# Optimization experiments

Measured on AMD Instinct MI355X. Metric: run time of the kernel, lower is better.

## Reference

```python
import jax, jax.numpy as jnp
import numpy as np

R = 32768          # number of human-object pairs
IN_FEATS = 3072    # input_size * 3 (person + object + union features)
HIDDEN = 1024      # input_size
NUM_CLASSES = 50   # action classes


def setup_inputs() -> dict:
    key = jax.random.key(0)
    k_x, k_w1, k_w2 = jax.random.split(key, 3)
    x = jax.random.normal(k_x, (R, IN_FEATS), dtype=jnp.float32)
    # Linear weights init: normal(std=0.01), bias 0 (as in the module)
    w1 = jax.random.normal(k_w1, (IN_FEATS, HIDDEN), dtype=jnp.float32) * 0.01
    b1 = jnp.zeros((HIDDEN,), dtype=jnp.float32)
    w2 = jax.random.normal(k_w2, (HIDDEN, NUM_CLASSES), dtype=jnp.float32) * 0.01
    b2 = jnp.zeros((NUM_CLASSES,), dtype=jnp.float32)
    return {"x": x, "w1": w1, "b1": b1, "w2": w2, "b2": b2}


def reference(x, w1, b1, w2, b2):
    # HoiOutputLayers.forward: scores = cls_score(relu(cls_fc1(x)))
    h = jax.nn.relu(jnp.dot(x, w1) + b1)          # [R, HIDDEN]
    scores = jnp.dot(h, w2) + b2                  # [R, NUM_CLASSES] action logits
    return scores
```

## Files before the change

### kernel.cpp

```cpp
#include <hip/hip_runtime.h>

#define K1 3072
#define N1 1024
#define NCOL 50

typedef float  f32x4  __attribute__((ext_vector_type(4)));
typedef short  short8 __attribute__((ext_vector_type(8)));

#define GLD16(g, l)                                                        \
  __builtin_amdgcn_global_load_lds(                                        \
      (const __attribute__((address_space(1))) void*)(g),                  \
      (__attribute__((address_space(3))) void*)(l), 16, 0, 0)

#define MFMA_BF16(a, b, c) __builtin_amdgcn_mfma_f32_16x16x32_bf16(a, b, c, 0, 0, 0)

__device__ inline unsigned bfr(float f) {
  return (__builtin_bit_cast(unsigned, f) + 0x8000u) >> 16;
}
__device__ inline short f2bf(float f) { return (short)bfr(f); }
__device__ inline short8 cvt8(float4 a, float4 b) {
  short8 r;
  r[0] = f2bf(a.x); r[1] = f2bf(a.y); r[2] = f2bf(a.z); r[3] = f2bf(a.w);
  r[4] = f2bf(b.x); r[5] = f2bf(b.y); r[6] = f2bf(b.z); r[7] = f2bf(b.w);
  return r;
}

__global__ __launch_bounds__(512) void xcvt_kernel(const float* __restrict__ X,
                                                   short* __restrict__ Xb) {
  size_t i = ((size_t)blockIdx.x * 512 + threadIdx.x) * 8;
  const size_t stride = (size_t)2048 * 512 * 8;
#pragma unroll 4
  for (int it = 0; it < 12; ++it, i += stride) {
    float4 u = *(const float4*)(X + i);
    float4 v = *(const float4*)(X + i + 4);
    *(short8*)(Xb + i) = cvt8(u, v);
  }
}

__global__ __launch_bounds__(256) void w1t_kernel(const float* __restrict__ W1,
                                                  short* __restrict__ W1T) {
  __shared__ float tile[64 * 65];
  const int t = threadIdx.x, b = blockIdx.x;
  const int k0 = (b >> 4) * 64, n0 = (b & 15) * 64;
#pragma unroll
  for (int i = 0; i < 16; ++i) {
    const int e = t + i * 256, r = e >> 6, c = e & 63;
    tile[r * 65 + c] = W1[(size_t)(k0 + r) * N1 + n0 + c];
  }
  __syncthreads();
#pragma unroll
  for (int i = 0; i < 16; ++i) {
    const int e = t + i * 256, kx = e & 63, ny = e >> 6;
    W1T[(size_t)(n0 + ny) * K1 + k0 + kx] = f2bf(tile[kx * 65 + ny]);
  }
}

__global__ __launch_bounds__(256) void w2t_kernel(const float* __restrict__ W2,
                                                  short* __restrict__ W2T) {
  const int idx = blockIdx.x * 256 + threadIdx.x;
  for (int e = idx; e < 64 * N1; e += 16 * 256) {
    const int c = e >> 10, k = e & 1023;
    const float v = (c < NCOL) ? W2[(size_t)k * NCOL + c] : 0.f;
    W2T[(size_t)c * N1 + k] = f2bf(v);
  }
}

#define BK2 64
#define NIT (K1 / BK2)
#define ASLOT (256 * 64)
#define SH2 264

struct __align__(16) Smem2 {
  union {
    struct { short A[2][ASLOT]; short B[2][ASLOT]; } s;
    struct { short h[128 * SH2]; short w2t[64 * SH2]; } e;
  } u;
};

__global__ __launch_bounds__(512, 2)
void hoi_fused2(const short* __restrict__ Xb, const short* __restrict__ W1T,
                const float* __restrict__ B1, const short* __restrict__ W2T,
                const float* __restrict__ B2, float* __restrict__ OUT) {
  __shared__ Smem2 sm;
  const int tid  = threadIdx.x;
  const int lane = tid & 63, wid = tid >> 6;
  const int wr = wid >> 2, wc = wid & 3;
  const int l15 = lane & 15, g = lane >> 4, l7 = l15 & 7;

  const int bid  = blockIdx.x;
  const int gidx = (bid & 7) * 64 + (bid >> 3);
  const int m_blk = gidx >> 2, n_blk = gidx & 3;
  const int m0 = m_blk * 256, n0 = n_blk * 256;

  const int srow  = lane >> 3;
  const int sslot = (lane & 7) ^ srow;
  const short* aS0 = Xb  + (size_t)(m0 + 0   + wid * 16 + srow) * K1 + sslot * 8;
  const short* aS1 = Xb  + (size_t)(m0 + 128 + wid * 16 + srow) * K1 + sslot * 8;
  const short* bS0 = W1T + (size_t)(n0 + 0   + wid * 16 + srow) * K1 + sslot * 8;
  const short* bS1 = W1T + (size_t)(n0 + 128 + wid * 16 + srow) * K1 + sslot * 8;
  const int dL0 = (0   + wid * 16) * 64;
  const int dL1 = (128 + wid * 16) * 64;

#define ISSUE_A0(kt, sl) do { GLD16(aS0 + (size_t)(kt) * BK2,                  &sm.u.s.A[sl][dL0]);        \
                              GLD16(aS0 + (size_t)8 * K1 + (size_t)(kt) * BK2, &sm.u.s.A[sl][dL0 + 512]); } while (0)
#define ISSUE_A1(kt, sl) do { GLD16(aS1 + (size_t)(kt) * BK2,                  &sm.u.s.A[sl][dL1]);        \
                              GLD16(aS1 + (size_t)8 * K1 + (size_t)(kt) * BK2, &sm.u.s.A[sl][dL1 + 512]); } while (0)
#define ISSUE_B0(kt, sl) do { GLD16(bS0 + (size_t)(kt) * BK2,                  &sm.u.s.B[sl][dL0]);        \
                              GLD16(bS0 + (size_t)8 * K1 + (size_t)(kt) * BK2, &sm.u.s.B[sl][dL0 + 512]); } while (0)
#define ISSUE_B1(kt, sl) do { GLD16(bS1 + (size_t)(kt) * BK2,                  &sm.u.s.B[sl][dL1]);        \
                              GLD16(bS1 + (size_t)8 * K1 + (size_t)(kt) * BK2, &sm.u.s.B[sl][dL1 + 512]); } while (0)

  const int aRd = (wr * 128 + l15) * 64;
  const int bRd = (wc * 64  + l15) * 64;
  const int sk0 = ((g)     ^ l7) * 8;
  const int sk1 = ((4 | g) ^ l7) * 8;

  float b1v[4];
#pragma unroll
  for (int nf = 0; nf < 4; ++nf) b1v[nf] = B1[n0 + wc * 64 + nf * 16 + l15];

  f32x4 acc[8][4] = {};

  ISSUE_A0(0, 0); ISSUE_A1(0, 0); ISSUE_B0(0, 0); ISSUE_B1(0, 0);

  for (int t = 0; t < NIT; ++t) {
    const int s  = t & 1, sx = s ^ 1;
    const int tn = (t + 1 < NIT) ? t + 1 : NIT - 1;

    __builtin_amdgcn_s_barrier();
    ISSUE_A0(tn, sx);
    __builtin_amdgcn_sched_barrier(0);
    asm volatile("s_waitcnt vmcnt(2)" ::: "memory");
    __builtin_amdgcn_s_barrier();
    __builtin_amdgcn_sched_barrier(0);
    ISSUE_A1(tn, sx);
    ISSUE_B0(tn, sx);
    ISSUE_B1(tn, sx);
    __builtin_amdgcn_sched_barrier(0);

    short8 a_[4][2], b_[4][2];

#pragma unroll
    for (int mf = 0; mf < 4; ++mf) {
      a_[mf][0] = *(const short8*)&sm.u.s.A[s][aRd + mf * 1024 + sk0];
      a_[mf][1] = *(const short8*)&sm.u.s.A[s][aRd + mf * 1024 + sk1];
    }
#pragma unroll
    for (int nf = 0; nf < 2; ++nf) {
      b_[nf][0] = *(const short8*)&sm.u.s.B[s][bRd + nf * 1024 + sk0];
      b_[nf][1] = *(const short8*)&sm.u.s.B[s][bRd + nf * 1024 + sk1];
    }
    asm volatile("s_waitcnt lgkmcnt(0)" ::: "memory");
    __builtin_amdgcn_sched_barrier(0);
    __builtin_amdgcn_s_setprio(1);
#pragma unroll
    for (int mf = 0; mf < 4; ++mf)
#pragma unroll
      for (int nf = 0; nf < 2; ++nf) {
        acc[mf][nf] = MFMA_BF16(a_[mf][0], b_[nf][0], acc[mf][nf]);
        acc[mf][nf] = MFMA_BF16(a_[mf][1], b_[nf][1], acc[mf][nf]);
      }
    __builtin_amdgcn_s_setprio(0);
    __builtin_amdgcn_sched_barrier(0);

#pragma unroll
    for (int nf = 2; nf < 4; ++nf) {
      b_[nf][0] = *(const short8*)&sm.u.s.B[s][bRd + nf * 1024 + sk0];
      b_[nf][1] = *(const short8*)&sm.u.s.B[s][bRd + nf * 1024 + sk1];
    }
    asm volatile("s_waitcnt lgkmcnt(0)" ::: "memory");
    __builtin_amdgcn_sched_barrier(0);
    __builtin_amdgcn_s_setprio(1);
#pragma unroll
    for (int mf = 0; mf < 4; ++mf)
#pragma unroll
      for (int nf = 2; nf < 4; ++nf) {
        acc[mf][nf] = MFMA_BF16(a_[mf][0], b_[nf][0], acc[mf][nf]);
        acc[mf][nf] = MFMA_BF16(a_[mf][1], b_[nf][1], acc[mf][nf]);
      }
    __builtin_amdgcn_s_setprio(0);
    __builtin_amdgcn_sched_barrier(0);

#pragma unroll
    for (int mf = 0; mf < 4; ++mf) {
      a_[mf][0] = *(const short8*)&sm.u.s.A[s][aRd + (4 + mf) * 1024 + sk0];
      a_[mf][1] = *(const short8*)&sm.u.s.A[s][aRd + (4 + mf) * 1024 + sk1];
    }
    asm volatile("s_waitcnt lgkmcnt(0)" ::: "memory");
    __builtin_amdgcn_sched_barrier(0);
    __builtin_amdgcn_s_setprio(1);
#pragma unroll
    for (int mf = 0; mf < 4; ++mf)
#pragma unroll
      for (int nf = 0; nf < 2; ++nf) {
        acc[4 + mf][nf] = MFMA_BF16(a_[mf][0], b_[nf][0], acc[4 + mf][nf]);
        acc[4 + mf][nf] = MFMA_BF16(a_[mf][1], b_[nf][1], acc[4 + mf][nf]);
      }
    __builtin_amdgcn_s_setprio(0);
    __builtin_amdgcn_sched_barrier(0);

    __builtin_amdgcn_s_setprio(1);
#pragma unroll
    for (int mf = 0; mf < 4; ++mf)
#pragma unroll
      for (int nf = 2; nf < 4; ++nf) {
        acc[4 + mf][nf] = MFMA_BF16(a_[mf][0], b_[nf][0], acc[4 + mf][nf]);
        acc[4 + mf][nf] = MFMA_BF16(a_[mf][1], b_[nf][1], acc[4 + mf][nf]);
      }
    __builtin_amdgcn_s_setprio(0);
  }
#undef ISSUE_A0
#undef ISSUE_A1
#undef ISSUE_B0
#undef ISSUE_B1

  for (int ph = 0; ph < 2; ++ph) {
    __syncthreads();

    if (wr == ph) {
#pragma unroll
      for (int mf = 0; mf < 8; ++mf)
#pragma unroll
        for (int nf = 0; nf < 4; ++nf) {
          const int c = wc * 64 + nf * 16 + l15;
#pragma unroll
          for (int j = 0; j < 4; ++j) {
            const int r = mf * 16 + g * 4 + j;
            sm.u.e.h[r * SH2 + c] = f2bf(fmaxf(acc[mf][nf][j] + b1v[nf], 0.f));
          }
        }
    }
    if (ph == 0) {
      const int c = tid & 63, part = tid >> 6;
#pragma unroll
      for (int i = 0; i < 4; ++i)
        *(short8*)&sm.u.e.w2t[c * SH2 + part * 32 + i * 8] =
            *(const short8*)&W2T[(size_t)c * N1 + n0 + part * 32 + i * 8];
    }
    __syncthreads();

    f32x4 acc2[4] = {};
#pragma unroll
    for (int ks = 0; ks < 8; ++ks) {
      const short8 a2 = *(const short8*)&sm.u.e.h[(wid * 16 + l15) * SH2 + ks * 32 + g * 8];
#pragma unroll
      for (int nt = 0; nt < 4; ++nt) {
        const short8 b2 = *(const short8*)&sm.u.e.w2t[(nt * 16 + l15) * SH2 + ks * 32 + g * 8];
        acc2[nt] = MFMA_BF16(a2, b2, acc2[nt]);
      }
    }
#pragma unroll
    for (int nt = 0; nt < 4; ++nt) {
      const int c = nt * 16 + l15;
      if (c < NCOL) {
#pragma unroll
        for (int j = 0; j < 4; ++j) {
          const int r = m0 + ph * 128 + wid * 16 + g * 4 + j;
          float v = acc2[nt][j];
          if (n_blk == 0) v += B2[c];
          atomicAdd(&OUT[(size_t)r * NCOL + c], v);
        }
      }
    }
  }
}

#define BK 32
#define NSTEP (K1 / BK)
#define SAS 40
#define SHS 136

struct __align__(16) Smem0 {
  union {
    struct { short A[128 * SAS]; short BT[128 * SAS]; } s[2];
    struct { short h[64 * SHS]; short w2t[64 * SHS]; } e;
  } u;
};

__global__ __launch_bounds__(256, 3)
void hoi_fused0(const float* __restrict__ X, const float* __restrict__ W1,
                const float* __restrict__ B1, const float* __restrict__ W2,
                const float* __restrict__ B2, float* __restrict__ OUT) {
  __shared__ Smem0 sm;
  const int tid  = threadIdx.x;
  const int lane = tid & 63, wid = tid >> 6;
  const int wr = wid >> 1, wc = wid & 1;
  const int l15 = lane & 15, g = lane >> 4;
  const int bid   = blockIdx.x;
  const int xcd   = bid & 7, o = bid >> 3;
  const int m_blk = xcd * 32 + (o >> 3);
  const int n_blk = o & 7;
  const int m0 = m_blk * 128, n0 = n_blk * 128;

  const int arow = tid >> 1;
  const int akc  = (tid & 1) << 4;
  const float* aptr = X + (size_t)(m0 + arow) * K1 + akc;
  const int bk2 = tid >> 4, bcm = tid & 15;
  const float* bptr = W1 + (size_t)(2 * bk2) * N1 + n0 + bcm;

  float b1v[4];
#pragma unroll
  for (int nt = 0; nt < 4; ++nt) b1v[nt] = B1[n0 + wc * 64 + nt * 16 + l15];

  f32x4 acc[4][4] = {};
  float4 ra[4];
  float  rb0[8], rb1[8];
#pragma unroll
  for (int q = 0; q < 4; ++q) ra[q] = *(const float4*)(aptr + 4 * q);
#pragma unroll
  for (int i = 0; i < 8; ++i) { rb0[i] = bptr[16 * i]; rb1[i] = bptr[N1 + 16 * i]; }

  for (int step = 0; step < NSTEP; ++step) {
    const int cb = step & 1;
    const short8 av0 = cvt8(ra[0], ra[1]);
    const short8 av1 = cvt8(ra[2], ra[3]);
    unsigned bpk[8];
#pragma unroll
    for (int i = 0; i < 8; ++i)
      bpk[i] = bfr(rb0[i]) | ((__builtin_bit_cast(unsigned, rb1[i]) + 0x8000u) & 0xFFFF0000u);
    if (step + 1 < NSTEP) {
      const int k0v = (step + 1) * BK;
#pragma unroll
      for (int q = 0; q < 4; ++q) ra[q] = *(const float4*)(aptr + k0v + 4 * q);
      const float* bp = bptr + (size_t)k0v * N1;
#pragma unroll
      for (int i = 0; i < 8; ++i) { rb0[i] = bp[16 * i]; rb1[i] = bp[N1 + 16 * i]; }
    }
    *(short8*)&sm.u.s[cb].A[arow * SAS + akc + 0] = av0;
    *(short8*)&sm.u.s[cb].A[arow * SAS + akc + 8] = av1;
#pragma unroll
    for (int i = 0; i < 8; ++i)
      *(unsigned*)&sm.u.s[cb].BT[(bcm + 16 * i) * SAS + 2 * bk2] = bpk[i];

    asm volatile("s_waitcnt lgkmcnt(0)" ::: "memory");
    __builtin_amdgcn_s_barrier();
    __builtin_amdgcn_sched_barrier(0);

    short8 af[4];
#pragma unroll
    for (int mt = 0; mt < 4; ++mt)
      af[mt] = *(const short8*)&sm.u.s[cb].A[(wr * 64 + mt * 16 + l15) * SAS + g * 8];
#pragma unroll
    for (int nt = 0; nt < 4; ++nt) {
      short8 bfv = *(const short8*)&sm.u.s[cb].BT[(wc * 64 + nt * 16 + l15) * SAS + g * 8];
#pragma unroll
      for (int mt = 0; mt < 4; ++mt)
        acc[mt][nt] = MFMA_BF16(af[mt], bfv, acc[mt][nt]);
    }
  }

  for (int p = 0; p < 2; ++p) {
    __syncthreads();
    if (wr == p) {
#pragma unroll
      for (int mt = 0; mt < 4; ++mt)
#pragma unroll
        for (int nt = 0; nt < 4; ++nt) {
          const int c = wc * 64 + nt * 16 + l15;
#pragma unroll
          for (int j = 0; j < 4; ++j) {
            const int r = mt * 16 + g * 4 + j;
            sm.u.e.h[r * SHS + c] = f2bf(fmaxf(acc[mt][nt][j] + b1v[nt], 0.f));
          }
        }
    }
    if (p == 0) {
      const int kk = tid >> 1, ch = (tid & 1) * 32;
#pragma unroll
      for (int i = 0; i < 32; ++i) {
        const int c = ch + i;
        const float v = (c < NCOL) ? W2[(size_t)(n0 + kk) * NCOL + c] : 0.f;
        sm.u.e.w2t[c * SHS + kk] = f2bf(v);
      }
    }
    __syncthreads();

    f32x4 acc2[4] = {};
#pragma unroll
    for (int ks = 0; ks < 4; ++ks) {
      const short8 a2f = *(const short8*)&sm.u.e.h[(wid * 16 + l15) * SHS + ks * 32 + g * 8];
#pragma unroll
      for (int nt2 = 0; nt2 < 4; ++nt2) {
        const short8 b2f = *(const short8*)&sm.u.e.w2t[(nt2 * 16 + l15) * SHS + ks * 32 + g * 8];
        acc2[nt2] = MFMA_BF16(a2f, b2f, acc2[nt2]);
      }
    }
#pragma unroll
    for (int nt2 = 0; nt2 < 4; ++nt2) {
      const int c = nt2 * 16 + l15;
      if (c < NCOL) {
#pragma unroll
        for (int j = 0; j < 4; ++j) {
          const int r = m0 + p * 64 + wid * 16 + g * 4 + j;
          float v = acc2[nt2][j];
          if (n_blk == 0) v += B2[c];
          atomicAdd(&OUT[(size_t)r * NCOL + c], v);
        }
      }
    }
  }
}

extern "C" void kernel_launch(void* const* d_in, const int* in_sizes, int n_in,
                              void* d_out, int out_size, void* d_ws, size_t ws_size,
                              hipStream_t stream) {
  const float* X  = (const float*)d_in[0];
  const float* W1 = (const float*)d_in[1];
  const float* B1 = (const float*)d_in[2];
  const float* W2 = (const float*)d_in[3];
  const float* B2 = (const float*)d_in[4];
  float* OUT = (float*)d_out;

  const size_t XB_BYTES  = (size_t)32768 * K1 * 2;
  const size_t W1T_BYTES = (size_t)N1 * K1 * 2;
  const size_t W2T_BYTES = (size_t)64 * N1 * 2;

  hipMemsetAsync(d_out, 0, (size_t)out_size * sizeof(float), stream);

  if (ws_size >= XB_BYTES + W1T_BYTES + W2T_BYTES) {
    short* Xb  = (short*)d_ws;
    short* W1T = (short*)((char*)d_ws + XB_BYTES);
    short* W2T = (short*)((char*)d_ws + XB_BYTES + W1T_BYTES);
    hipLaunchKernelGGL(xcvt_kernel, dim3(2048), dim3(512), 0, stream, X, Xb);
    hipLaunchKernelGGL(w1t_kernel, dim3(768), dim3(256), 0, stream, W1, W1T);
    hipLaunchKernelGGL(w2t_kernel, dim3(16), dim3(256), 0, stream, W2, W2T);
    hipLaunchKernelGGL(hoi_fused2, dim3(512), dim3(512), 0, stream, Xb, W1T, B1, W2T, B2, OUT);
  } else {
    hipLaunchKernelGGL(hoi_fused0, dim3(2048), dim3(256), 0, stream, X, W1, B1, W2, B2, OUT);
  }
}
```

Before: 340.4 us.

## Interleave global-to-LDS prefetch issues across MFMA phases with finer barriers

Reassigns which rows each wave loads so the A and B tiles split into four quarter-chunks, each issued between the four MFMA phases of the main loop rather than all at the top of the iteration. Per-phase vmcnt waits and workgroup barriers are added so each chunk is known complete before the next iteration reads it. The aim is to spread memory issue evenly across compute and hide load latency behind MFMAs. The cost is many more s_barrier syncs per iteration, which could add stalls.

```diff
diff --git a/kernel.cpp b/kernel.cpp
--- a/kernel.cpp
+++ b/kernel.cpp
@@ -13,6 +13,7 @@
       (__attribute__((address_space(3))) void*)(l), 16, 0, 0)
 
 #define MFMA_BF16(a, b, c) __builtin_amdgcn_mfma_f32_16x16x32_bf16(a, b, c, 0, 0, 0)
+#define SBAR()  __builtin_amdgcn_sched_barrier(0)
 
 __device__ inline unsigned bfr(float f) {
   return (__builtin_bit_cast(unsigned, f) + 0x8000u) >> 16;
@@ -94,21 +95,26 @@
 
   const int srow  = lane >> 3;
   const int sslot = (lane & 7) ^ srow;
-  const short* aS0 = Xb  + (size_t)(m0 + 0   + wid * 16 + srow) * K1 + sslot * 8;
-  const short* aS1 = Xb  + (size_t)(m0 + 128 + wid * 16 + srow) * K1 + sslot * 8;
-  const short* bS0 = W1T + (size_t)(n0 + 0   + wid * 16 + srow) * K1 + sslot * 8;
-  const short* bS1 = W1T + (size_t)(n0 + 128 + wid * 16 + srow) * K1 + sslot * 8;
-  const int dL0 = (0   + wid * 16) * 64;
-  const int dL1 = (128 + wid * 16) * 64;
-
-#define ISSUE_A0(kt, sl) do { GLD16(aS0 + (size_t)(kt) * BK2,                  &sm.u.s.A[sl][dL0]);        \
-                              GLD16(aS0 + (size_t)8 * K1 + (size_t)(kt) * BK2, &sm.u.s.A[sl][dL0 + 512]); } while (0)
-#define ISSUE_A1(kt, sl) do { GLD16(aS1 + (size_t)(kt) * BK2,                  &sm.u.s.A[sl][dL1]);        \
-                              GLD16(aS1 + (size_t)8 * K1 + (size_t)(kt) * BK2, &sm.u.s.A[sl][dL1 + 512]); } while (0)
-#define ISSUE_B0(kt, sl) do { GLD16(bS0 + (size_t)(kt) * BK2,                  &sm.u.s.B[sl][dL0]);        \
-                              GLD16(bS0 + (size_t)8 * K1 + (size_t)(kt) * BK2, &sm.u.s.B[sl][dL0 + 512]); } while (0)
-#define ISSUE_B1(kt, sl) do { GLD16(bS1 + (size_t)(kt) * BK2,                  &sm.u.s.B[sl][dL1]);        \
-                              GLD16(bS1 + (size_t)8 * K1 + (size_t)(kt) * BK2, &sm.u.s.B[sl][dL1 + 512]); } while (0)
+
+  const int uj0 = 2 * wid, uj1 = 2 * wid + 1;
+  const int arA_0 = (uj0 >> 3) * 128 + (uj0 & 7) * 8;
+  const int arA_1 = (uj1 >> 3) * 128 + (uj1 & 7) * 8;
+  const int brB_0 = (uj0 >> 2) * 64 + (uj0 & 3) * 8;
+  const int brB_1 = (uj1 >> 2) * 64 + (uj1 & 3) * 8;
+
+  const short* aP0 = Xb  + (size_t)(m0 + arA_0 + srow) * K1 + sslot * 8;
+  const short* aP1 = Xb  + (size_t)(m0 + arA_1 + srow) * K1 + sslot * 8;
+  const short* bP0 = W1T + (size_t)(n0 + brB_0 + srow) * K1 + sslot * 8;
+  const short* bP1 = W1T + (size_t)(n0 + brB_1 + srow) * K1 + sslot * 8;
+
+#define ISSUE_A0(kt, sl) do { GLD16(aP0 + (size_t)(kt) * BK2,                   &sm.u.s.A[sl][arA_0 * 64]);        \
+                              GLD16(aP1 + (size_t)(kt) * BK2,                   &sm.u.s.A[sl][arA_1 * 64]); } while (0)
+#define ISSUE_A1(kt, sl) do { GLD16(aP0 + (size_t)64 * K1 + (size_t)(kt) * BK2, &sm.u.s.A[sl][arA_0 * 64 + 4096]); \
+                              GLD16(aP1 + (size_t)64 * K1 + (size_t)(kt) * BK2, &sm.u.s.A[sl][arA_1 * 64 + 4096]); } while (0)
+#define ISSUE_B0(kt, sl) do { GLD16(bP0 + (size_t)(kt) * BK2,                   &sm.u.s.B[sl][brB_0 * 64]);        \
+                              GLD16(bP1 + (size_t)(kt) * BK2,                   &sm.u.s.B[sl][brB_1 * 64]); } while (0)
+#define ISSUE_B1(kt, sl) do { GLD16(bP0 + (size_t)32 * K1 + (size_t)(kt) * BK2, &sm.u.s.B[sl][brB_0 * 64 + 2048]); \
+                              GLD16(bP1 + (size_t)32 * K1 + (size_t)(kt) * BK2, &sm.u.s.B[sl][brB_1 * 64 + 2048]); } while (0)
 
   const int aRd = (wr * 128 + l15) * 64;
   const int bRd = (wc * 64  + l15) * 64;
@@ -121,23 +127,18 @@
 
   f32x4 acc[8][4] = {};
 
-  ISSUE_A0(0, 0); ISSUE_A1(0, 0); ISSUE_B0(0, 0); ISSUE_B1(0, 0);
+  ISSUE_A0(0, 0); SBAR();
+  ISSUE_B0(0, 0); SBAR();
+  ISSUE_B1(0, 0); SBAR();
+  ISSUE_A1(0, 0); SBAR();
+  asm volatile("s_waitcnt vmcnt(4)" ::: "memory");
+  __builtin_amdgcn_s_barrier();
+  SBAR();
 
   for (int t = 0; t < NIT; ++t) {
     const int s  = t & 1, sx = s ^ 1;
     const int tn = (t + 1 < NIT) ? t + 1 : NIT - 1;
 
-    __builtin_amdgcn_s_barrier();
-    ISSUE_A0(tn, sx);
-    __builtin_amdgcn_sched_barrier(0);
-    asm volatile("s_waitcnt vmcnt(2)" ::: "memory");
-    __builtin_amdgcn_s_barrier();
-    __builtin_amdgcn_sched_barrier(0);
-    ISSUE_A1(tn, sx);
-    ISSUE_B0(tn, sx);
-    ISSUE_B1(tn, sx);
-    __builtin_amdgcn_sched_barrier(0);
-
     short8 a_[4][2], b_[4][2];
 
 #pragma unroll
@@ -150,8 +151,11 @@
       b_[nf][0] = *(const short8*)&sm.u.s.B[s][bRd + nf * 1024 + sk0];
       b_[nf][1] = *(const short8*)&sm.u.s.B[s][bRd + nf * 1024 + sk1];
     }
+    ISSUE_A0(tn, sx);
+    SBAR();
+    __builtin_amdgcn_s_barrier();
     asm volatile("s_waitcnt lgkmcnt(0)" ::: "memory");
-    __builtin_amdgcn_sched_barrier(0);
+    SBAR();
     __builtin_amdgcn_s_setprio(1);
 #pragma unroll
     for (int mf = 0; mf < 4; ++mf)
@@ -161,15 +165,21 @@
         acc[mf][nf] = MFMA_BF16(a_[mf][1], b_[nf][1], acc[mf][nf]);
       }
     __builtin_amdgcn_s_setprio(0);
-    __builtin_amdgcn_sched_barrier(0);
+    asm volatile("s_waitcnt vmcnt(4)" ::: "memory");
+    SBAR();
+    __builtin_amdgcn_s_barrier();
+    SBAR();
 
 #pragma unroll
     for (int nf = 2; nf < 4; ++nf) {
       b_[nf][0] = *(const short8*)&sm.u.s.B[s][bRd + nf * 1024 + sk0];
       b_[nf][1] = *(const short8*)&sm.u.s.B[s][bRd + nf * 1024 + sk1];
     }
+    ISSUE_B0(tn, sx);
+    SBAR();
+    __builtin_amdgcn_s_barrier();
     asm volatile("s_waitcnt lgkmcnt(0)" ::: "memory");
-    __builtin_amdgcn_sched_barrier(0);
+    SBAR();
     __builtin_amdgcn_s_setprio(1);
 #pragma unroll
     for (int mf = 0; mf < 4; ++mf)
@@ -179,15 +189,21 @@
         acc[mf][nf] = MFMA_BF16(a_[mf][1], b_[nf][1], acc[mf][nf]);
       }
     __builtin_amdgcn_s_setprio(0);
-    __builtin_amdgcn_sched_barrier(0);
+    asm volatile("s_waitcnt vmcnt(4)" ::: "memory");
+    SBAR();
+    __builtin_amdgcn_s_barrier();
+    SBAR();
 
 #pragma unroll
     for (int mf = 0; mf < 4; ++mf) {
       a_[mf][0] = *(const short8*)&sm.u.s.A[s][aRd + (4 + mf) * 1024 + sk0];
       a_[mf][1] = *(const short8*)&sm.u.s.A[s][aRd + (4 + mf) * 1024 + sk1];
     }
+    ISSUE_B1(tn, sx);
+    SBAR();
+    __builtin_amdgcn_s_barrier();
     asm volatile("s_waitcnt lgkmcnt(0)" ::: "memory");
-    __builtin_amdgcn_sched_barrier(0);
+    SBAR();
     __builtin_amdgcn_s_setprio(1);
 #pragma unroll
     for (int mf = 0; mf < 4; ++mf)
@@ -197,8 +213,13 @@
         acc[4 + mf][nf] = MFMA_BF16(a_[mf][1], b_[nf][1], acc[4 + mf][nf]);
       }
     __builtin_amdgcn_s_setprio(0);
-    __builtin_amdgcn_sched_barrier(0);
-
+    SBAR();
+    __builtin_amdgcn_s_barrier();
+    SBAR();
+
+    ISSUE_A1(tn, sx);
+    SBAR();
+    __builtin_amdgcn_s_barrier();
     __builtin_amdgcn_s_setprio(1);
 #pragma unroll
     for (int mf = 0; mf < 4; ++mf)
@@ -208,6 +229,10 @@
         acc[4 + mf][nf] = MFMA_BF16(a_[mf][1], b_[nf][1], acc[4 + mf][nf]);
       }
     __builtin_amdgcn_s_setprio(0);
+    asm volatile("s_waitcnt vmcnt(4)" ::: "memory");
+    SBAR();
+    __builtin_amdgcn_s_barrier();
+    SBAR();
   }
 #undef ISSUE_A0
 #undef ISSUE_A1
```

Measured after the change: 340.5 us. No clear change (+0.0%).

## Double waves per block and halve per-wave tile in fused HOI GEMM

Applied to the files above, without the earlier changes.

Launches the fused GEMM with 1024 threads (16 waves) instead of 512. The block still covers a 256x256 output tile, but each wave now owns a 64x64 sub-tile with half the accumulators. Global-to-LDS staging is redistributed so each wave issues one 16-byte load per operand half. The second-layer epilogue is split across more waves. The aim is more resident waves to hide memory and LDS latency, at the cost of more LDS fragment reads per MFMA and less register-level reuse.

```diff
diff --git a/kernel.cpp b/kernel.cpp
--- a/kernel.cpp
+++ b/kernel.cpp
@@ -13,6 +13,7 @@
       (__attribute__((address_space(3))) void*)(l), 16, 0, 0)
 
 #define MFMA_BF16(a, b, c) __builtin_amdgcn_mfma_f32_16x16x32_bf16(a, b, c, 0, 0, 0)
+#define SBAR()  __builtin_amdgcn_sched_barrier(0)
 
 __device__ inline unsigned bfr(float f) {
   return (__builtin_bit_cast(unsigned, f) + 0x8000u) >> 16;
@@ -77,8 +78,8 @@
   } u;
 };
 
-__global__ __launch_bounds__(512, 2)
-void hoi_fused2(const short* __restrict__ Xb, const short* __restrict__ W1T,
+__global__ __launch_bounds__(1024, 4)
+void hoi_fused3(const short* __restrict__ Xb, const short* __restrict__ W1T,
                 const float* __restrict__ B1, const short* __restrict__ W2T,
                 const float* __restrict__ B2, float* __restrict__ OUT) {
   __shared__ Smem2 sm;
@@ -94,24 +95,17 @@
 
   const int srow  = lane >> 3;
   const int sslot = (lane & 7) ^ srow;
-  const short* aS0 = Xb  + (size_t)(m0 + 0   + wid * 16 + srow) * K1 + sslot * 8;
-  const short* aS1 = Xb  + (size_t)(m0 + 128 + wid * 16 + srow) * K1 + sslot * 8;
-  const short* bS0 = W1T + (size_t)(n0 + 0   + wid * 16 + srow) * K1 + sslot * 8;
-  const short* bS1 = W1T + (size_t)(n0 + 128 + wid * 16 + srow) * K1 + sslot * 8;
-  const int dL0 = (0   + wid * 16) * 64;
-  const int dL1 = (128 + wid * 16) * 64;
-
-#define ISSUE_A0(kt, sl) do { GLD16(aS0 + (size_t)(kt) * BK2,                  &sm.u.s.A[sl][dL0]);        \
-                              GLD16(aS0 + (size_t)8 * K1 + (size_t)(kt) * BK2, &sm.u.s.A[sl][dL0 + 512]); } while (0)
-#define ISSUE_A1(kt, sl) do { GLD16(aS1 + (size_t)(kt) * BK2,                  &sm.u.s.A[sl][dL1]);        \
-                              GLD16(aS1 + (size_t)8 * K1 + (size_t)(kt) * BK2, &sm.u.s.A[sl][dL1 + 512]); } while (0)
-#define ISSUE_B0(kt, sl) do { GLD16(bS0 + (size_t)(kt) * BK2,                  &sm.u.s.B[sl][dL0]);        \
-                              GLD16(bS0 + (size_t)8 * K1 + (size_t)(kt) * BK2, &sm.u.s.B[sl][dL0 + 512]); } while (0)
-#define ISSUE_B1(kt, sl) do { GLD16(bS1 + (size_t)(kt) * BK2,                  &sm.u.s.B[sl][dL1]);        \
-                              GLD16(bS1 + (size_t)8 * K1 + (size_t)(kt) * BK2, &sm.u.s.B[sl][dL1 + 512]); } while (0)
-
-  const int aRd = (wr * 128 + l15) * 64;
-  const int bRd = (wc * 64  + l15) * 64;
+  const short* aP = Xb  + (size_t)(m0 + wid * 8 + srow) * K1 + sslot * 8;
+  const short* bP = W1T + (size_t)(n0 + wid * 8 + srow) * K1 + sslot * 8;
+  const int dA = (wid * 8) * 64;
+
+#define I_A0(kt, sl) GLD16(aP + (size_t)(kt) * BK2,                    &sm.u.s.A[sl][dA])
+#define I_A1(kt, sl) GLD16(aP + (size_t)128 * K1 + (size_t)(kt) * BK2, &sm.u.s.A[sl][dA + 8192])
+#define I_B0(kt, sl) GLD16(bP + (size_t)(kt) * BK2,                    &sm.u.s.B[sl][dA])
+#define I_B1(kt, sl) GLD16(bP + (size_t)128 * K1 + (size_t)(kt) * BK2, &sm.u.s.B[sl][dA + 8192])
+
+  const int aRd = (wr * 64 + l15) * 64;
+  const int bRd = (wc * 64 + l15) * 64;
   const int sk0 = ((g)     ^ l7) * 8;
   const int sk1 = ((4 | g) ^ l7) * 8;
 
@@ -119,144 +113,121 @@
 #pragma unroll
   for (int nf = 0; nf < 4; ++nf) b1v[nf] = B1[n0 + wc * 64 + nf * 16 + l15];
 
-  f32x4 acc[8][4] = {};
-
-  ISSUE_A0(0, 0); ISSUE_A1(0, 0); ISSUE_B0(0, 0); ISSUE_B1(0, 0);
+  f32x4 acc[4][4] = {};
+
+  I_A0(0, 0); I_B0(0, 0); I_B1(0, 0); I_A1(0, 0);
+  asm volatile("s_waitcnt vmcnt(0)" ::: "memory");
+  __builtin_amdgcn_s_barrier();
 
   for (int t = 0; t < NIT; ++t) {
     const int s  = t & 1, sx = s ^ 1;
     const int tn = (t + 1 < NIT) ? t + 1 : NIT - 1;
 
     __builtin_amdgcn_s_barrier();
-    ISSUE_A0(tn, sx);
-    __builtin_amdgcn_sched_barrier(0);
-    asm volatile("s_waitcnt vmcnt(2)" ::: "memory");
+    I_A0(tn, sx);
+    SBAR();
+    asm volatile("s_waitcnt vmcnt(1)" ::: "memory");
     __builtin_amdgcn_s_barrier();
-    __builtin_amdgcn_sched_barrier(0);
-    ISSUE_A1(tn, sx);
-    ISSUE_B0(tn, sx);
-    ISSUE_B1(tn, sx);
-    __builtin_amdgcn_sched_barrier(0);
-
-    short8 a_[4][2], b_[4][2];
-
-#pragma unroll
-    for (int mf = 0; mf < 4; ++mf) {
+    SBAR();
+    I_A1(tn, sx);
+    I_B0(tn, sx);
+    I_B1(tn, sx);
+    SBAR();
+
+    short8 a_[2][2], b_[4][2];
+
+#pragma unroll
+    for (int mf = 0; mf < 2; ++mf) {
       a_[mf][0] = *(const short8*)&sm.u.s.A[s][aRd + mf * 1024 + sk0];
       a_[mf][1] = *(const short8*)&sm.u.s.A[s][aRd + mf * 1024 + sk1];
     }
 #pragma unroll
-    for (int nf = 0; nf < 2; ++nf) {
+    for (int nf = 0; nf < 4; ++nf) {
       b_[nf][0] = *(const short8*)&sm.u.s.B[s][bRd + nf * 1024 + sk0];
       b_[nf][1] = *(const short8*)&sm.u.s.B[s][bRd + nf * 1024 + sk1];
     }
     asm volatile("s_waitcnt lgkmcnt(0)" ::: "memory");
-    __builtin_amdgcn_sched_barrier(0);
+    SBAR();
     __builtin_amdgcn_s_setprio(1);
 #pragma unroll
-    for (int mf = 0; mf < 4; ++mf)
-#pragma unroll
-      for (int nf = 0; nf < 2; ++nf) {
+    for (int mf = 0; mf < 2; ++mf)
+#pragma unroll
+      for (int nf = 0; nf < 4; ++nf) {
         acc[mf][nf] = MFMA_BF16(a_[mf][0], b_[nf][0], acc[mf][nf]);
         acc[mf][nf] = MFMA_BF16(a_[mf][1], b_[nf][1], acc[mf][nf]);
       }
     __builtin_amdgcn_s_setprio(0);
-    __builtin_amdgcn_sched_barrier(0);
-
-#pragma unroll
-    for (int nf = 2; nf < 4; ++nf) {
-      b_[nf][0] = *(const short8*)&sm.u.s.B[s][bRd + nf * 1024 + sk0];
-      b_[nf][1] = *(const short8*)&sm.u.s.B[s][bRd + nf * 1024 + sk1];
+    SBAR();
+
+#pragma unroll
+    for (int mf = 0; mf < 2; ++mf) {
+      a_[mf][0] = *(const short8*)&sm.u.s.A[s][aRd + (2 + mf) * 1024 + sk0];
+      a_[mf][1] = *(const short8*)&sm.u.s.A[s][aRd + (2 + mf) * 1024 + sk1];
     }
     asm volatile("s_waitcnt lgkmcnt(0)" ::: "memory");
-    __builtin_amdgcn_sched_barrier(0);
+    SBAR();
     __builtin_amdgcn_s_setprio(1);
 #pragma unroll
-    for (int mf = 0; mf < 4; ++mf)
-#pragma unroll
-      for (int nf = 2; nf < 4; ++nf) {
-        acc[mf][nf] = MFMA_BF16(a_[mf][0], b_[nf][0], acc[mf][nf]);
-        acc[mf][nf] = MFMA_BF16(a_[mf][1], b_[nf][1], acc[mf][nf]);
+    for (int mf = 0; mf < 2; ++mf)
+#pragma unroll
+      for (int nf = 0; nf < 4; ++nf) {
+        acc[2 + mf][nf] = MFMA_BF16(a_[mf][0], b_[nf][0], acc[2 + mf][nf]);
+        acc[2 + mf][nf] = MFMA_BF16(a_[mf][1], b_[nf][1], acc[2 + mf][nf]);
       }
     __builtin_amdgcn_s_setprio(0);
-    __builtin_amdgcn_sched_barrier(0);
-
-#pragma unroll
-    for (int mf = 0; mf < 4; ++mf) {
-      a_[mf][0] = *(const short8*)&sm.u.s.A[s][aRd + (4 + mf) * 1024 + sk0];
-      a_[mf][1] = *(const short8*)&sm.u.s.A[s][aRd + (4 + mf) * 1024 + sk1];
-    }
-    asm volatile("s_waitcnt lgkmcnt(0)" ::: "memory");
-    __builtin_amdgcn_sched_barrier(0);
-    __builtin_amdgcn_s_setprio(1);
-#pragma unroll
-    for (int mf = 0; mf < 4; ++mf)
-#pragma unroll
-      for (int nf = 0; nf < 2; ++nf) {
-        acc[4 + mf][nf] = MFMA_BF16(a_[mf][0], b_[nf][0], acc[4 + mf][nf]);
-        acc[4 + mf][nf] = MFMA_BF16(a_[mf][1], b_[nf][1], acc[4 + mf][nf]);
-      }
-    __builtin_amdgcn_s_setprio(0);
-    __builtin_amdgcn_sched_barrier(0);
-
-    __builtin_amdgcn_s_setprio(1);
-#pragma unroll
-    for (int mf = 0; mf < 4; ++mf)
-#pragma unroll
-      for (int nf = 2; nf < 4; ++nf) {
-        acc[4 + mf][nf] = MFMA_BF16(a_[mf][0], b_[nf][0], acc[4 + mf][nf]);
-        acc[4 + mf][nf] = MFMA_BF16(a_[mf][1], b_[nf][1], acc[4 + mf][nf]);
-      }
-    __builtin_amdgcn_s_setprio(0);
-  }
-#undef ISSUE_A0
-#undef ISSUE_A1
-#undef ISSUE_B0
-#undef ISSUE_B1
+    SBAR();
+  }
+#undef I_A0
+#undef I_A1
+#undef I_B0
+#undef I_B1
 
   for (int ph = 0; ph < 2; ++ph) {
     __syncthreads();
 
-    if (wr == ph) {
-#pragma unroll
-      for (int mf = 0; mf < 8; ++mf)
+    if ((wr >> 1) == ph) {
+      const int rbase = (wr & 1) * 64;
+#pragma unroll
+      for (int mf = 0; mf < 4; ++mf)
 #pragma unroll
         for (int nf = 0; nf < 4; ++nf) {
           const int c = wc * 64 + nf * 16 + l15;
 #pragma unroll
           for (int j = 0; j < 4; ++j) {
-            const int r = mf * 16 + g * 4 + j;
+            const int r = rbase + mf * 16 + g * 4 + j;
             sm.u.e.h[r * SH2 + c] = f2bf(fmaxf(acc[mf][nf][j] + b1v[nf], 0.f));
           }
         }
     }
     if (ph == 0) {
-      const int c = tid & 63, part = tid >> 6;
-#pragma unroll
-      for (int i = 0; i < 4; ++i)
-        *(short8*)&sm.u.e.w2t[c * SH2 + part * 32 + i * 8] =
-            *(const short8*)&W2T[(size_t)c * N1 + n0 + part * 32 + i * 8];
+      const int c = tid >> 4, k0c = (tid & 15) * 16;
+      *(short8*)&sm.u.e.w2t[c * SH2 + k0c + 0] =
+          *(const short8*)&W2T[(size_t)c * N1 + n0 + k0c + 0];
+      *(short8*)&sm.u.e.w2t[c * SH2 + k0c + 8] =
+          *(const short8*)&W2T[(size_t)c * N1 + n0 + k0c + 8];
     }
     __syncthreads();
 
-    f32x4 acc2[4] = {};
+    const int rg = wid >> 1, nh = wid & 1;
+    f32x4 acc2[2] = {};
 #pragma unroll
     for (int ks = 0; ks < 8; ++ks) {
-      const short8 a2 = *(const short8*)&sm.u.e.h[(wid * 16 + l15) * SH2 + ks * 32 + g * 8];
-#pragma unroll
-      for (int nt = 0; nt < 4; ++nt) {
-        const short8 b2 = *(const short8*)&sm.u.e.w2t[(nt * 16 + l15) * SH2 + ks * 32 + g * 8];
-        acc2[nt] = MFMA_BF16(a2, b2, acc2[nt]);
-      }
-    }
-#pragma unroll
-    for (int nt = 0; nt < 4; ++nt) {
-      const int c = nt * 16 + l15;
+      const short8 a2 = *(const short8*)&sm.u.e.h[(rg * 16 + l15) * SH2 + ks * 32 + g * 8];
+#pragma unroll
+      for (int nfl = 0; nfl < 2; ++nfl) {
+        const short8 b2 =
+            *(const short8*)&sm.u.e.w2t[(nh * 32 + nfl * 16 + l15) * SH2 + ks * 32 + g * 8];
+        acc2[nfl] = MFMA_BF16(a2, b2, acc2[nfl]);
+      }
+    }
+#pragma unroll
+    for (int nfl = 0; nfl < 2; ++nfl) {
+      const int c = nh * 32 + nfl * 16 + l15;
       if (c < NCOL) {
 #pragma unroll
         for (int j = 0; j < 4; ++j) {
-          const int r = m0 + ph * 128 + wid * 16 + g * 4 + j;
-          float v = acc2[nt][j];
+          const int r = m0 + ph * 128 + rg * 16 + g * 4 + j;
+          float v = acc2[nfl][j];
           if (n_blk == 0) v += B2[c];
           atomicAdd(&OUT[(size_t)r * NCOL + c], v);
         }
@@ -424,7 +395,7 @@
     hipLaunchKernelGGL(xcvt_kernel, dim3(2048), dim3(512), 0, stream, X, Xb);
     hipLaunchKernelGGL(w1t_kernel, dim3(768), dim3(256), 0, stream, W1, W1T);
     hipLaunchKernelGGL(w2t_kernel, dim3(16), dim3(256), 0, stream, W2, W2T);
-    hipLaunchKernelGGL(hoi_fused2, dim3(512), dim3(512), 0, stream, Xb, W1T, B1, W2T, B2, OUT);
+    hipLaunchKernelGGL(hoi_fused3, dim3(512), dim3(1024), 0, stream, Xb, W1T, B1, W2T, B2, OUT);
   } else {
     hipLaunchKernelGGL(hoi_fused0, dim3(2048), dim3(256), 0, stream, X, W1, B1, W2, B2, OUT);
   }
```

Result: faster. 327.5 us, median of 3 (-3.8%).
